# Kernel tuning notes

Measured on AMD Instinct MI355X. Metric: run time of the kernel, lower is better.

Reference implementation:

```python
import jax, jax.numpy as jnp
import numpy as np

R = 3            # window radius -> (2R+1)^2 = 49 neighbors
N = 128          # grid side, n
K = 131          # 3 + 64 + 64 channels
C = 21           # num_classes
B = 2            # batch
W = (2 * R + 1) ** 2


def setup_inputs() -> dict:
    key = jax.random.key(0)
    k1, k2, k3, k4 = jax.random.split(key, 4)
    return {
        "intergrated": jax.random.normal(k1, (B, K, N, N), jnp.float32),
        "x2": jax.random.normal(k2, (B, C, N * N), jnp.float32),
        "sel_mask": jax.random.randint(k3, (B, N, N), 0, 2).astype(jnp.int32),
        "conv_parameter": jax.random.uniform(k4, (K,), jnp.float32),
    }


def _shifts(x, r):
    """Gather (2r+1)^2 shifted copies: x [..., n, n] -> [..., n, n, W].
    Entry w=(di,dj) holds x[i+di-r, j+dj-r] (zero-padded out of bounds)."""
    n = x.shape[-1]
    pad = [(0, 0)] * (x.ndim - 2) + [(r, r), (r, r)]
    xp = jnp.pad(x, pad)
    cols = [xp[..., di:di + n, dj:dj + n]
            for di in range(2 * r + 1) for dj in range(2 * r + 1)]
    return jnp.stack(cols, axis=-1)


def _rwn_single(feats, x2b, maskb, conv_parameter):
    """feats [K,n,n], x2b [C,n^2], maskb [n,n] int -> y [n^2, C]."""
    n = feats.shape[-1]
    m = maskb.astype(feats.dtype)            # sampled-pixel indicator
    xm = feats * m                            # sparse-sampled features [K,n,n]
    nbr = _shifts(xm, R)                      # [K,n,n,W] neighbor values
    valid = _shifts(jnp.ones((n, n), feats.dtype), R) > 0  # [n,n,W] in-bounds
    # per-channel windowed L1 distance, exp, per-pixel normalization (softmax
    # of +distance over the valid window, as in the original code)
    d = jnp.abs(xm[..., None] - nbr)          # [K,n,n,W]
    e = jnp.where(valid[None], jnp.exp(d), 0.0)
    a = e / e.sum(axis=-1, keepdims=True)     # rows sum to 1 per channel
    # W = sum_k conv_parameter[k] * a_k, rows only for selected pixels
    A = jnp.einsum('k,kijw->ijw', conv_parameter, a) * m[..., None]  # [n,n,W]
    # y[q,c] = sum_p W[p,q] * x2[p,c]  (W^T @ x2^T, per original col/row swap)
    feat = x2b.reshape(C, n, n)
    msg = A[None] * feat[..., None]           # [C,n,n,W]
    ypad = jnp.zeros((C, n + 2 * R, n + 2 * R), feats.dtype)
    w = 0
    for di in range(2 * R + 1):
        for dj in range(2 * R + 1):
            ypad = ypad.at[:, di:di + n, dj:dj + n].add(msg[..., w])
            w += 1
    y = ypad[:, R:R + n, R:R + n].reshape(C, n * n)
    return y.T                                 # [n^2, C]


def reference(intergrated, x2, sel_mask, conv_parameter):
    f = lambda fe, xb, mb: _rwn_single(fe, xb, mb, conv_parameter)
    return jax.vmap(f)(intergrated, x2, sel_mask)  # [B, n^2, C]
```

## Files before the change

kernel.cpp:

```cpp
#include <hip/hip_runtime.h>
#include <hip/hip_fp16.h>

#define R_ 3
#define D_ 7
#define W_ 49
#define N_ 128
#define K_ 131
#define C_ 21
#define B_ 2
#define NN (N_ * N_)
#define TI_ 8
#define TJ_ 16
#define PROWS (TI_ + 2 * R_)
#define PCOLS (TJ_ + 2 * R_)
#define PSTR 24
#define NELEM (PROWS * PCOLS)
#define LDSP (PROWS * PSTR + 8)
#define KC 8
#define KCHUNK ((K_ + KC - 1) / KC)
#define HCELLS (PROWS * PCOLS)

typedef __fp16 h2 __attribute__((ext_vector_type(2)));

static __device__ __forceinline__ unsigned h2u(h2 x) { return __builtin_bit_cast(unsigned, x); }
static __device__ __forceinline__ h2 u2h(unsigned x) { return __builtin_bit_cast(h2, x); }

#if defined(__has_builtin)
#if __has_builtin(__builtin_amdgcn_fdot2)
#define FDOT2(a, b, c) __builtin_amdgcn_fdot2((a), (b), (c), false)
#endif
#endif
#ifndef FDOT2
#define FDOT2(a, b, c) ((c) + (float)(a)[0] * (float)(b)[0] + (float)(a)[1] * (float)(b)[1])
#endif

__global__ __launch_bounds__(256) void rwn_affinity(
    const float* __restrict__ feats,
    const int*   __restrict__ mask,
    const float* __restrict__ cp,
    float* __restrict__ Aout)
{
    __shared__ unsigned patchw[LDSP];

    const int tile = blockIdx.x;
    const int kc   = blockIdx.y;
    const int b    = blockIdx.z;
    const int tr = tile >> 3, tc = tile & 7;
    const int ti0 = tr * TI_, tj0 = tc * TJ_;

    const int tid = threadIdx.x;
    const int pix = tid >> 1;
    const int h   = tid & 1;
    const int ti = pix >> 4;
    const int tj = pix & 15;
    const int gi = ti0 + ti, gj = tj0 + tj;

    const float LOG2E = 1.4426950408889634f;
    int   soff[2];
    float swt[2];
    float ozw[2];
    int   slds[2];
    #pragma unroll
    for (int r = 0; r < 2; ++r) {
        int e = tid + r * 256;
        bool act = (e < NELEM);
        int pr = e / PCOLS, pc = e - pr * PCOLS;
        int mi = ti0 + pr - R_, mj = tj0 + pc - R_;
        bool inb = act && mi >= 0 && mi < N_ && mj >= 0 && mj < N_;
        int cmi = mi < 0 ? 0 : (mi > N_ - 1 ? N_ - 1 : mi);
        int cmj = mj < 0 ? 0 : (mj > N_ - 1 ? N_ - 1 : mj);
        soff[r] = cmi * N_ + cmj;
        swt[r]  = inb ? ((float)mask[b * NN + soff[r]] * LOG2E) : 0.f;
        ozw[r]  = inb ? 1.f : 0.f;
        slds[r] = act ? (pr * PSTR + pc) : (PROWS * PSTR + 4);
    }

    const h2 ph2 = h ? (h2){(__fp16)1.f, (__fp16)0.f}
                     : (h2){(__fp16)1.f, (__fp16)1.f};
    const h2 one2 = (h2){(__fp16)1.f, (__fp16)1.f};
    const int cbase = (ti + R_) * PSTR + (tj + R_);
    const int bh = ti * PSTR + tj + 4 * h;

    h2 Aacc[14];
    #pragma unroll
    for (int i = 0; i < 14; ++i) Aacc[i] = (h2){(__fp16)0.f, (__fp16)0.f};

    const int k0 = kc * KCHUNK;
    const int k1 = (k0 + KCHUNK < K_) ? (k0 + KCHUNK) : K_;
    const float* fb = feats + (size_t)b * K_ * NN;

    for (int e = tid; e < LDSP; e += 256) patchw[e] = 0u;

    const float* fk0 = fb + (size_t)k0 * NN;
    float pre0 = fk0[soff[0]] * swt[0];
    float pre1 = fk0[soff[1]] * swt[1];

    __syncthreads();

    for (int k = k0; k < k1; ++k) {
        patchw[slds[0]] = h2u(__builtin_amdgcn_cvt_pkrtz(ozw[0] * exp2f(pre0),
                                                         ozw[0] * exp2f(-pre0)));
        patchw[slds[1]] = h2u(__builtin_amdgcn_cvt_pkrtz(ozw[1] * exp2f(pre1),
                                                         ozw[1] * exp2f(-pre1)));
        float n0 = 0.f, n1 = 0.f;
        if (k + 1 < k1) {
            const float* fn = fb + (size_t)(k + 1) * NN;
            n0 = fn[soff[0]] * swt[0];
            n1 = fn[soff[1]] * swt[1];
        }
        __syncthreads();

        const unsigned cw = patchw[cbase];
        const h2 cE2 = u2h(__builtin_amdgcn_perm(cw, cw, 0x01000100u));
        const h2 cI2 = u2h(__builtin_amdgcn_perm(cw, cw, 0x03020302u));

        h2 ex[14];
        float dsum = 0.f;
        #pragma unroll
        for (int u = 0; u < D_; ++u) {
            const int rb = bh + u * PSTR;
            const unsigned w0 = patchw[rb];
            const unsigned w1 = patchw[rb + 1];
            const unsigned w2 = patchw[rb + 2];
            const unsigned w3 = patchw[rb + 3];
            const h2 E01 = u2h(__builtin_amdgcn_perm(w1, w0, 0x05040100u));
            const h2 I01 = u2h(__builtin_amdgcn_perm(w1, w0, 0x07060302u));
            const h2 E23 = u2h(__builtin_amdgcn_perm(w3, w2, 0x05040100u));
            const h2 I23 = u2h(__builtin_amdgcn_perm(w3, w2, 0x07060302u));
            h2 t01 = __builtin_elementwise_max(cE2 * I01, E01 * cI2);
            h2 t23 = __builtin_elementwise_max(cE2 * I23, E23 * cI2);
            t23 = t23 * ph2;
            dsum = FDOT2(t01, one2, dsum);
            dsum = FDOT2(t23, one2, dsum);
            ex[u * 2]     = t01;
            ex[u * 2 + 1] = t23;
        }
        const float denom = dsum + __shfl_xor(dsum, 1, 64);
        const float scale = cp[k] * __frcp_rn(denom);
        const h2 s2 = __builtin_amdgcn_cvt_pkrtz(scale, scale);
        #pragma unroll
        for (int m = 0; m < 14; ++m) Aacc[m] = ex[m] * s2 + Aacc[m];
        __syncthreads();

        pre0 = n0; pre1 = n1;
    }

    if (mask[b * NN + gi * N_ + gj] != 0) {
        const int pixg = gi * N_ + gj;
        float* ab = Aout + (size_t)b * W_ * NN + pixg;
        #pragma unroll
        for (int u = 0; u < D_; ++u) {
            #pragma unroll
            for (int m = 0; m < 2; ++m) {
                const h2 tv = Aacc[u * 2 + m];
                const int wbase = u * D_ + 4 * h + 2 * m;
                atomicAdd(ab + (size_t)wbase * NN, (float)tv[0]);
                if (h == 0 || m < 1)
                    atomicAdd(ab + (size_t)(wbase + 1) * NN, (float)tv[1]);
            }
        }
    }
}

__global__ __launch_bounds__(512) void rwn_gather(
    const float* __restrict__ Aarr,
    const float* __restrict__ x2,
    float* __restrict__ out)
{
    __shared__ float x2h[C_ * HCELLS];

    const int tile = blockIdx.x;
    const int b    = blockIdx.y;
    const int tr = tile >> 3, tc = tile & 7;
    const int gi0 = tr * TI_, gj0 = tc * TJ_;

    const int tid = threadIdx.x;

    const float* xb = x2 + (size_t)b * C_ * NN;
    for (int e = tid; e < C_ * HCELLS; e += 512) {
        const int c = e / HCELLS, cell = e - c * HCELLS;
        const int pr = cell / PCOLS, pc = cell - pr * PCOLS;
        const int mi = gi0 + pr - R_, mj = gj0 + pc - R_;
        const bool inb = (mi >= 0 && mi < N_ && mj >= 0 && mj < N_);
        const int cmi = mi < 0 ? 0 : (mi > N_ - 1 ? N_ - 1 : mi);
        const int cmj = mj < 0 ? 0 : (mj > N_ - 1 ? N_ - 1 : mj);
        x2h[e] = inb ? xb[c * NN + cmi * N_ + cmj] : 0.f;
    }
    __syncthreads();

    const int h = tid & 3;
    const int q = tid >> 2;
    const int qi = q >> 4, qj = q & 15;
    const int gi = gi0 + qi, gj = gj0 + qj;
    const float* Ab = Aarr + (size_t)b * W_ * NN;

    float av[13];
    int   cells[13];
    #pragma unroll
    for (int idx = 0; idx < 13; ++idx) {
        int w = h + 4 * idx;
        const float valid = (w < W_) ? 1.f : 0.f;
        if (w >= W_) w = W_ - 1;
        const int u = w / D_, v = w - u * D_;
        const int pi = gi + R_ - u, pj = gj + R_ - v;
        const int cmi = pi < 0 ? 0 : (pi > N_ - 1 ? N_ - 1 : pi);
        const int cmj = pj < 0 ? 0 : (pj > N_ - 1 ? N_ - 1 : pj);
        av[idx]    = valid * Ab[(size_t)w * NN + cmi * N_ + cmj];
        cells[idx] = (qi + 2 * R_ - u) * PCOLS + (qj + 2 * R_ - v);
    }

    float acc[C_];
    #pragma unroll
    for (int c = 0; c < C_; ++c) acc[c] = 0.f;
    #pragma unroll
    for (int idx = 0; idx < 13; ++idx) {
        const float a = av[idx];
        const float* xc = x2h + cells[idx];
        #pragma unroll
        for (int c = 0; c < C_; ++c)
            acc[c] += a * xc[c * HCELLS];
    }

    #pragma unroll
    for (int c = 0; c < C_; ++c) {
        acc[c] += __shfl_xor(acc[c], 1, 64);
        acc[c] += __shfl_xor(acc[c], 2, 64);
    }

    __syncthreads();
    if (h == 0) {
        float* os = x2h + q * C_;
        #pragma unroll
        for (int c = 0; c < C_; ++c) os[c] = acc[c];
    }
    __syncthreads();
    for (int e = tid; e < TI_ * TJ_ * C_; e += 512) {
        const int qq = e / C_, cc = e - qq * C_;
        const int gq = (gi0 + (qq >> 4)) * N_ + gj0 + (qq & 15);
        out[((size_t)b * NN + gq) * C_ + cc] = x2h[e];
    }
}

extern "C" void kernel_launch(void* const* d_in, const int* in_sizes, int n_in,
                              void* d_out, int out_size, void* d_ws, size_t ws_size,
                              hipStream_t stream) {
    const float* feats = (const float*)d_in[0];
    const float* x2    = (const float*)d_in[1];
    const int*   mask  = (const int*)d_in[2];
    const float* cp    = (const float*)d_in[3];
    float* out = (float*)d_out;

    float* Aarr = (float*)d_ws;
    const size_t Abytes = (size_t)B_ * W_ * NN * sizeof(float);

    (void)hipMemsetAsync(Aarr, 0, Abytes, stream);

    dim3 gridA(128, KC, B_);
    rwn_affinity<<<gridA, 256, 0, stream>>>(feats, mask, cp, Aarr);

    dim3 gridG(128, B_);
    rwn_gather<<<gridG, 512, 0, stream>>>(Aarr, x2, out);
}
```

Measured before the change: 149.1 us.

## Replace atomic accumulation with per-chunk fp16 slot buffers reduced in gather

The affinity kernel no longer atomically adds each K-chunk's partial weights into one fp32 array. It now writes packed fp16 partials into a separate slot buffer per chunk, zeroing unselected pixels, and the gather kernel sums the eight chunks as it reads. This drops the memset and the contended float atomics. In exchange the workspace is larger, the gather reads more data, and the partial sums are stored at fp16 precision. The old atomic path is kept as a fallback for when the workspace is too small.

```diff
diff --git a/kernel.cpp b/kernel.cpp
--- a/kernel.cpp
+++ b/kernel.cpp
@@ -19,6 +19,7 @@
 #define KC 8
 #define KCHUNK ((K_ + KC - 1) / KC)
 #define HCELLS (PROWS * PCOLS)
+#define NSLOT 28
 
 typedef __fp16 h2 __attribute__((ext_vector_type(2)));
 
@@ -34,11 +35,11 @@
 #define FDOT2(a, b, c) ((c) + (float)(a)[0] * (float)(b)[0] + (float)(a)[1] * (float)(b)[1])
 #endif
 
-__global__ __launch_bounds__(256) void rwn_affinity(
+__global__ __launch_bounds__(256) void rwn_affinity_s(
     const float* __restrict__ feats,
     const int*   __restrict__ mask,
     const float* __restrict__ cp,
-    float* __restrict__ Aout)
+    unsigned* __restrict__ Asl)
 {
     __shared__ unsigned patchw[LDSP];
 
@@ -145,6 +146,198 @@
         pre0 = n0; pre1 = n1;
     }
 
+    const int mk = mask[b * NN + gi * N_ + gj];
+    const h2 z2 = (h2){(__fp16)0.f, (__fp16)0.f};
+    const int pixg = gi * N_ + gj;
+    unsigned* ab = Asl + ((size_t)(kc * B_ + b) * NSLOT) * NN + pixg;
+    #pragma unroll
+    for (int u = 0; u < D_; ++u) {
+        #pragma unroll
+        for (int m = 0; m < 2; ++m) {
+            const h2 tv = mk ? Aacc[u * 2 + m] : z2;
+            ab[(size_t)(u * 4 + 2 * h + m) * NN] = h2u(tv);
+        }
+    }
+}
+
+__global__ __launch_bounds__(512) void rwn_gather_s(
+    const unsigned* __restrict__ Asl,
+    const float* __restrict__ x2,
+    float* __restrict__ out)
+{
+    __shared__ float x2h[C_ * HCELLS];
+
+    const int tile = blockIdx.x;
+    const int b    = blockIdx.y;
+    const int tr = tile >> 3, tc = tile & 7;
+    const int gi0 = tr * TI_, gj0 = tc * TJ_;
+
+    const int tid = threadIdx.x;
+
+    const float* xb = x2 + (size_t)b * C_ * NN;
+    for (int e = tid; e < C_ * HCELLS; e += 512) {
+        const int c = e / HCELLS, cell = e - c * HCELLS;
+        const int pr = cell / PCOLS, pc = cell - pr * PCOLS;
+        const int mi = gi0 + pr - R_, mj = gj0 + pc - R_;
+        const bool inb = (mi >= 0 && mi < N_ && mj >= 0 && mj < N_);
+        const int cmi = mi < 0 ? 0 : (mi > N_ - 1 ? N_ - 1 : mi);
+        const int cmj = mj < 0 ? 0 : (mj > N_ - 1 ? N_ - 1 : mj);
+        x2h[e] = inb ? xb[c * NN + cmi * N_ + cmj] : 0.f;
+    }
+    __syncthreads();
+
+    const int h = tid & 3;
+    const int q = tid >> 2;
+    const int qi = q >> 4, qj = q & 15;
+    const int gi = gi0 + qi, gj = gj0 + qj;
+
+    float av[13];
+    int   cells[13];
+    #pragma unroll
+    for (int idx = 0; idx < 13; ++idx) {
+        int w = h + 4 * idx;
+        const float valid0 = (w < W_) ? 1.f : 0.f;
+        if (w >= W_) w = 0;
+        const int u = w / D_, vv = w - u * D_;
+        const int s = vv >> 1, ln = vv & 1;
+        const int pi = gi + R_ - u, pj = gj + R_ - vv;
+        const int cmi = pi < 0 ? 0 : (pi > N_ - 1 ? N_ - 1 : pi);
+        const int cmj = pj < 0 ? 0 : (pj > N_ - 1 ? N_ - 1 : pj);
+        const float valid = (pi >= 0 && pi < N_ && pj >= 0 && pj < N_)
+                          ? valid0 : 0.f;
+        const int p = cmi * N_ + cmj;
+        const size_t wordoff = (size_t)(u * 4 + s) * NN + p;
+        float alo = 0.f, ahi = 0.f;
+        #pragma unroll
+        for (int kc = 0; kc < KC; ++kc) {
+            const h2 pr2 = u2h(Asl[((size_t)(kc * B_ + b) * NSLOT) * NN + wordoff]);
+            alo += (float)pr2[0];
+            ahi += (float)pr2[1];
+        }
+        av[idx]    = valid * (ln ? ahi : alo);
+        cells[idx] = (qi + 2 * R_ - u) * PCOLS + (qj + 2 * R_ - vv);
+    }
+
+    float acc[C_];
+    #pragma unroll
+    for (int c = 0; c < C_; ++c) acc[c] = 0.f;
+    #pragma unroll
+    for (int idx = 0; idx < 13; ++idx) {
+        const float a = av[idx];
+        const float* xc = x2h + cells[idx];
+        #pragma unroll
+        for (int c = 0; c < C_; ++c)
+            acc[c] += a * xc[c * HCELLS];
+    }
+
+    #pragma unroll
+    for (int c = 0; c < C_; ++c) {
+        acc[c] += __shfl_xor(acc[c], 1, 64);
+        acc[c] += __shfl_xor(acc[c], 2, 64);
+    }
+
+    __syncthreads();
+    if (h == 0) {
+        float* os = x2h + q * C_;
+        #pragma unroll
+        for (int c = 0; c < C_; ++c) os[c] = acc[c];
+    }
+    __syncthreads();
+    for (int e = tid; e < TI_ * TJ_ * C_; e += 512) {
+        const int qq = e / C_, cc = e - qq * C_;
+        const int gq = (gi0 + (qq >> 4)) * N_ + gj0 + (qq & 15);
+        out[((size_t)b * NN + gq) * C_ + cc] = x2h[e];
+    }
+}
+
+__global__ __launch_bounds__(256) void rwn_affinity_at(
+    const float* __restrict__ feats, const int* __restrict__ mask,
+    const float* __restrict__ cp, float* __restrict__ Aout)
+{
+    __shared__ unsigned patchw[LDSP];
+    const int tile = blockIdx.x, kc = blockIdx.y, b = blockIdx.z;
+    const int tr = tile >> 3, tc = tile & 7;
+    const int ti0 = tr * TI_, tj0 = tc * TJ_;
+    const int tid = threadIdx.x;
+    const int pix = tid >> 1, h = tid & 1;
+    const int ti = pix >> 4, tj = pix & 15;
+    const int gi = ti0 + ti, gj = tj0 + tj;
+    const float LOG2E = 1.4426950408889634f;
+    int soff[2]; float swt[2]; float ozw[2]; int slds[2];
+    #pragma unroll
+    for (int r = 0; r < 2; ++r) {
+        int e = tid + r * 256;
+        bool act = (e < NELEM);
+        int pr = e / PCOLS, pc = e - pr * PCOLS;
+        int mi = ti0 + pr - R_, mj = tj0 + pc - R_;
+        bool inb = act && mi >= 0 && mi < N_ && mj >= 0 && mj < N_;
+        int cmi = mi < 0 ? 0 : (mi > N_ - 1 ? N_ - 1 : mi);
+        int cmj = mj < 0 ? 0 : (mj > N_ - 1 ? N_ - 1 : mj);
+        soff[r] = cmi * N_ + cmj;
+        swt[r]  = inb ? ((float)mask[b * NN + soff[r]] * LOG2E) : 0.f;
+        ozw[r]  = inb ? 1.f : 0.f;
+        slds[r] = act ? (pr * PSTR + pc) : (PROWS * PSTR + 4);
+    }
+    const h2 ph2 = h ? (h2){(__fp16)1.f, (__fp16)0.f}
+                     : (h2){(__fp16)1.f, (__fp16)1.f};
+    const h2 one2 = (h2){(__fp16)1.f, (__fp16)1.f};
+    const int cbase = (ti + R_) * PSTR + (tj + R_);
+    const int bh = ti * PSTR + tj + 4 * h;
+    h2 Aacc[14];
+    #pragma unroll
+    for (int i = 0; i < 14; ++i) Aacc[i] = (h2){(__fp16)0.f, (__fp16)0.f};
+    const int k0 = kc * KCHUNK;
+    const int k1 = (k0 + KCHUNK < K_) ? (k0 + KCHUNK) : K_;
+    const float* fb = feats + (size_t)b * K_ * NN;
+    for (int e = tid; e < LDSP; e += 256) patchw[e] = 0u;
+    const float* fk0 = fb + (size_t)k0 * NN;
+    float pre0 = fk0[soff[0]] * swt[0];
+    float pre1 = fk0[soff[1]] * swt[1];
+    __syncthreads();
+    for (int k = k0; k < k1; ++k) {
+        patchw[slds[0]] = h2u(__builtin_amdgcn_cvt_pkrtz(ozw[0] * exp2f(pre0),
+                                                         ozw[0] * exp2f(-pre0)));
+        patchw[slds[1]] = h2u(__builtin_amdgcn_cvt_pkrtz(ozw[1] * exp2f(pre1),
+                                                         ozw[1] * exp2f(-pre1)));
+        float n0 = 0.f, n1 = 0.f;
+        if (k + 1 < k1) {
+            const float* fn = fb + (size_t)(k + 1) * NN;
+            n0 = fn[soff[0]] * swt[0];
+            n1 = fn[soff[1]] * swt[1];
+        }
+        __syncthreads();
+        const unsigned cw = patchw[cbase];
+        const h2 cE2 = u2h(__builtin_amdgcn_perm(cw, cw, 0x01000100u));
+        const h2 cI2 = u2h(__builtin_amdgcn_perm(cw, cw, 0x03020302u));
+        h2 ex[14];
+        float dsum = 0.f;
+        #pragma unroll
+        for (int u = 0; u < D_; ++u) {
+            const int rb = bh + u * PSTR;
+            const unsigned w0 = patchw[rb];
+            const unsigned w1 = patchw[rb + 1];
+            const unsigned w2 = patchw[rb + 2];
+            const unsigned w3 = patchw[rb + 3];
+            const h2 E01 = u2h(__builtin_amdgcn_perm(w1, w0, 0x05040100u));
+            const h2 I01 = u2h(__builtin_amdgcn_perm(w1, w0, 0x07060302u));
+            const h2 E23 = u2h(__builtin_amdgcn_perm(w3, w2, 0x05040100u));
+            const h2 I23 = u2h(__builtin_amdgcn_perm(w3, w2, 0x07060302u));
+            h2 t01 = __builtin_elementwise_max(cE2 * I01, E01 * cI2);
+            h2 t23 = __builtin_elementwise_max(cE2 * I23, E23 * cI2);
+            t23 = t23 * ph2;
+            dsum = FDOT2(t01, one2, dsum);
+            dsum = FDOT2(t23, one2, dsum);
+            ex[u * 2]     = t01;
+            ex[u * 2 + 1] = t23;
+        }
+        const float denom = dsum + __shfl_xor(dsum, 1, 64);
+        const float scale = cp[k] * __frcp_rn(denom);
+        const h2 s2 = __builtin_amdgcn_cvt_pkrtz(scale, scale);
+        #pragma unroll
+        for (int m = 0; m < 14; ++m) Aacc[m] = ex[m] * s2 + Aacc[m];
+        __syncthreads();
+        pre0 = n0; pre1 = n1;
+    }
     if (mask[b * NN + gi * N_ + gj] != 0) {
         const int pixg = gi * N_ + gj;
         float* ab = Aout + (size_t)b * W_ * NN + pixg;
@@ -162,20 +355,15 @@
     }
 }
 
-__global__ __launch_bounds__(512) void rwn_gather(
-    const float* __restrict__ Aarr,
-    const float* __restrict__ x2,
+__global__ __launch_bounds__(512) void rwn_gather_at(
+    const float* __restrict__ Aarr, const float* __restrict__ x2,
     float* __restrict__ out)
 {
     __shared__ float x2h[C_ * HCELLS];
-
-    const int tile = blockIdx.x;
-    const int b    = blockIdx.y;
+    const int tile = blockIdx.x, b = blockIdx.y;
     const int tr = tile >> 3, tc = tile & 7;
     const int gi0 = tr * TI_, gj0 = tc * TJ_;
-
     const int tid = threadIdx.x;
-
     const float* xb = x2 + (size_t)b * C_ * NN;
     for (int e = tid; e < C_ * HCELLS; e += 512) {
         const int c = e / HCELLS, cell = e - c * HCELLS;
@@ -187,13 +375,11 @@
         x2h[e] = inb ? xb[c * NN + cmi * N_ + cmj] : 0.f;
     }
     __syncthreads();
-
     const int h = tid & 3;
     const int q = tid >> 2;
     const int qi = q >> 4, qj = q & 15;
     const int gi = gi0 + qi, gj = gj0 + qj;
     const float* Ab = Aarr + (size_t)b * W_ * NN;
-
     float av[13];
     int   cells[13];
     #pragma unroll
@@ -208,7 +394,6 @@
         av[idx]    = valid * Ab[(size_t)w * NN + cmi * N_ + cmj];
         cells[idx] = (qi + 2 * R_ - u) * PCOLS + (qj + 2 * R_ - v);
     }
-
     float acc[C_];
     #pragma unroll
     for (int c = 0; c < C_; ++c) acc[c] = 0.f;
@@ -220,13 +405,11 @@
         for (int c = 0; c < C_; ++c)
             acc[c] += a * xc[c * HCELLS];
     }
-
     #pragma unroll
     for (int c = 0; c < C_; ++c) {
         acc[c] += __shfl_xor(acc[c], 1, 64);
         acc[c] += __shfl_xor(acc[c], 2, 64);
     }
-
     __syncthreads();
     if (h == 0) {
         float* os = x2h + q * C_;
@@ -250,14 +433,21 @@
     const float* cp    = (const float*)d_in[3];
     float* out = (float*)d_out;
 
-    float* Aarr = (float*)d_ws;
-    const size_t Abytes = (size_t)B_ * W_ * NN * sizeof(float);
-
-    (void)hipMemsetAsync(Aarr, 0, Abytes, stream);
-
-    dim3 gridA(128, KC, B_);
-    rwn_affinity<<<gridA, 256, 0, stream>>>(feats, mask, cp, Aarr);
-
-    dim3 gridG(128, B_);
-    rwn_gather<<<gridG, 512, 0, stream>>>(Aarr, x2, out);
+    const size_t need = (size_t)KC * B_ * NSLOT * NN * sizeof(unsigned);
+
+    if (ws_size >= need) {
+        unsigned* Asl = (unsigned*)d_ws;
+        dim3 gridA(128, KC, B_);
+        rwn_affinity_s<<<gridA, 256, 0, stream>>>(feats, mask, cp, Asl);
+        dim3 gridG(128, B_);
+        rwn_gather_s<<<gridG, 512, 0, stream>>>(Asl, x2, out);
+    } else {
+        float* Aarr = (float*)d_ws;
+        const size_t Abytes = (size_t)B_ * W_ * NN * sizeof(float);
+        (void)hipMemsetAsync(Aarr, 0, Abytes, stream);
+        dim3 gridA(128, KC, B_);
+        rwn_affinity_at<<<gridA, 256, 0, stream>>>(feats, mask, cp, Aarr);
+        dim3 gridG(128, B_);
+        rwn_gather_at<<<gridG, 512, 0, stream>>>(Aarr, x2, out);
+    }
 }
```

New measurement: 138.3 us. 7.2% less time.
